# Performance work log

Hardware: AMD Instinct MI355X
Metric: run time of the kernel (lower is better)

Reference implementation:

```python
import jax, jax.numpy as jnp
import numpy as np

NALGOS = 64
NTASKS = 256
SEQLEN = 4096


def setup_inputs() -> dict:
    key = jax.random.key(0)
    k1, k2, k3, k4, k5, k6 = jax.random.split(key, 6)
    lx = jax.random.randint(k1, (SEQLEN,), 0, NTASKS)
    task_matrix = jax.random.uniform(k2, (NTASKS, NTASKS), jnp.float32) * 2.0 - 1.0
    # positive, bounded away from zero (module clamps difficulty to >= 0)
    task_difficulty = jax.random.uniform(k3, (NTASKS,), jnp.float32) + 0.5
    alg_efficiency = 0.5 + 0.02 * jax.random.normal(k4, (NALGOS,), jnp.float32)
    alg_memory = 0.5 + 0.10 * jax.random.normal(k5, (NALGOS,), jnp.float32)
    alg_experience_boost = 0.5 + 0.02 * jax.random.normal(k6, (NALGOS,), jnp.float32)
    return {
        "lx": lx,
        "task_matrix": task_matrix,
        "task_difficulty": task_difficulty,
        "alg_efficiency": alg_efficiency,
        "alg_memory": alg_memory,
        "alg_experience_boost": alg_experience_boost,
    }


def _custom_sigmoid(x):
    # 2*exp(x)/(exp(x)+1) - 1  ==  2*sigmoid(x) - 1 (stable form)
    return 2.0 * jax.nn.sigmoid(x) - 1.0


def reference(lx, task_matrix, task_difficulty, alg_efficiency, alg_memory,
              alg_experience_boost):
    nalgos = alg_efficiency.shape[0]
    ntasks = task_matrix.shape[0]
    task_difficulty_scale = 1.0
    difficulty = task_difficulty * task_difficulty_scale  # (T,)

    mem = alg_memory[:, None]              # (A, 1)
    eff = alg_efficiency[:, None]          # (A, 1)
    boost = alg_experience_boost[:, None]  # (A, 1)

    def step(carry, t):
        res, sig = carry                   # each (A, T)
        tm_row = task_matrix[t][None, :]   # (1, T): transfer from current task t
        sig_task = sig[:, t][:, None]      # (A, 1): prior perf on current task
        new_res = res * mem + tm_row * (eff + sig_task * boost)
        new_sig = _custom_sigmoid(new_res / difficulty[None, :])
        return (new_res, new_sig), new_sig

    init = (jnp.zeros((nalgos, ntasks), task_matrix.dtype),
            jnp.zeros((nalgos, ntasks), task_matrix.dtype))
    _, sigs = jax.lax.scan(step, init, lx)        # (S, A, T)
    sigs = jnp.moveaxis(sigs, 0, -1)              # (A, T, S)
    # prepend the zero initial state at timestep 0 -> (A, T, S+1)
    zero0 = jnp.zeros((nalgos, ntasks, 1), sigs.dtype)
    return jnp.concatenate([zero0, sigs], axis=-1)
```

## Files before the change

kernel.cpp:

```cpp
#include <hip/hip_runtime.h>

#define SEQ 4096
#define NT  256
#define NA  64
#define NCKPT 16
#define LOG2E 1.4426950408889634f

__device__ __forceinline__ float rdlanef(float v, int l) {
    return __int_as_float(__builtin_amdgcn_readlane(__float_as_int(v), l));
}

__global__ __launch_bounds__(64) void k_chain(
    const int* __restrict__ lx, const float* __restrict__ tm,
    const float* __restrict__ diff, const float* __restrict__ eff_p,
    const float* __restrict__ mem_p, const float* __restrict__ boost_p,
    float* __restrict__ gbuf, float* __restrict__ ckpt)
{
    __shared__ int   s_lx[SEQ + 8];
    __shared__ float s_res[NT];
    const int lane = threadIdx.x;
    const int a = blockIdx.x;

    for (int i = lane; i < SEQ; i += 64) s_lx[i] = lx[i];
    if (lane < 8) s_lx[SEQ + lane] = lx[SEQ - 1];
    *(float4*)&s_res[4 * lane] = make_float4(0.f, 0.f, 0.f, 0.f);
    __syncthreads();

    const float eff   = eff_p[a];
    const float mem   = mem_p[a];
    const float boost = boost_p[a];
    const float A  = eff + boost;
    const float Bc = -2.0f * boost;

    float mpow = 1.0f, bb = mem;
    {
        const int n = 63 - lane;
#pragma unroll
        for (int k = 0; k < 6; ++k) { if (n & (1 << k)) mpow *= bb; bb *= bb; }
    }
    const float m64 = bb;

    float4 res = make_float4(0.0f, 0.0f, 0.0f, 0.0f);
    float g = eff;
    float garr = g;
    float T[64];

    int   vrow  = s_lx[lane];
    int   vcol  = s_lx[1 + lane];
    float klane = LOG2E / diff[vcol];
    float D = 0.0f;
#pragma unroll
    for (int i = 0; i < 64; ++i) {
        const int r = __builtin_amdgcn_readlane(vrow, i);
        T[i] = klane * tm[r * NT + vcol];
    }

    for (int B = 0; B < SEQ; B += 64) {
#pragma unroll
        for (int j = 0; j < 64; ++j) {
            garr = (lane == j) ? g : garr;
            const float tg = T[j] * g;
            D = fmaf(mem, D, tg);
            const float pb = rdlanef(D, j);
            const float q  = __builtin_amdgcn_rcpf(
                                 __builtin_amdgcn_exp2f(pb) + 1.0f);
            g = fmaf(Bc, q, A);
        }
        gbuf[a * SEQ + B + lane] = garr;

        const int Bn = B + 64;
        const bool last = (Bn >= SEQ);

        int vrow_n = vrow, vcol_n = vcol; float klane_n = klane;
        if (!last) {
            vrow_n  = s_lx[Bn + lane];
            vcol_n  = s_lx[Bn + 1 + lane];
            klane_n = LOG2E / diff[vcol_n];
#pragma unroll
            for (int i = 0; i < 64; ++i) {
                const int r = __builtin_amdgcn_readlane(vrow_n, i);
                T[i] = klane_n * tm[r * NT + vcol_n];
            }
        }

        const float w = garr * mpow;
        res.x *= m64; res.y *= m64; res.z *= m64; res.w *= m64;
        float4 pf[16];
#pragma unroll
        for (int d = 0; d < 16; ++d) {
            const int r = __builtin_amdgcn_readlane(vrow, d);
            pf[d] = *(const float4*)(tm + r * NT + 4 * lane);
        }
#pragma unroll
        for (int i = 0; i < 64; ++i) {
            const float sw = rdlanef(w, i);
            const float4 row = pf[i & 15];
            res.x = fmaf(sw, row.x, res.x);
            res.y = fmaf(sw, row.y, res.y);
            res.z = fmaf(sw, row.z, res.z);
            res.w = fmaf(sw, row.w, res.w);
            if (i < 48) {
                const int r = __builtin_amdgcn_readlane(vrow, i + 16);
                pf[i & 15] = *(const float4*)(tm + r * NT + 4 * lane);
            }
        }
        if ((Bn & 255) == 0)
            *(float4*)(ckpt + (a * NCKPT + (B >> 8)) * NT + 4 * lane) = res;

        if (!last) {
            __syncthreads();
            *(float4*)&s_res[4 * lane] = res;
            __syncthreads();
            const float R = s_res[vcol_n];
            D = klane_n * R;
            vrow = vrow_n; vcol = vcol_n; klane = klane_n;
        }
    }
}

__global__ __launch_bounds__(64) void k_out(
    const int* __restrict__ lx, const float* __restrict__ tm,
    const float* __restrict__ diff, const float* __restrict__ mem_p,
    const float* __restrict__ gbuf, const float* __restrict__ ckpt,
    float* __restrict__ out)
{
    __shared__ int   s_lx[256 + 8];
    __shared__ float s_g[256];
    __shared__ float s_tile[64 * 65];

    const int lane = threadIdx.x;
    const int b = blockIdx.x;
    const int a     = b >> 6;
    const int cg    = (b >> 4) & 3;
    const int chunk = b & 15;
    const int t0 = chunk << 8;

    for (int i = lane; i < 256; i += 64) {
        s_lx[i] = lx[t0 + i];
        s_g[i]  = gbuf[a * SEQ + t0 + i];
    }
    if (lane < 8) s_lx[256 + lane] = lx[t0 + 255];
    __syncthreads();

    const int c = (cg << 6) + lane;
    const float memv = mem_p[a];
    const float kc = LOG2E / diff[c];
    float res = (chunk == 0) ? 0.0f
                             : ckpt[(a * NCKPT + chunk - 1) * NT + c];

    float pf[8];
#pragma unroll
    for (int d = 0; d < 8; ++d) pf[d] = tm[s_lx[d] * NT + c];

    const long rowbase = (long)(a * NT + (cg << 6)) * (SEQ + 1);
    for (int jb = 0; jb < 256; jb += 64) {
        const int   vpfl = s_lx[jb + 8 + lane];
        const float vg   = s_g[jb + lane];
        for (int j0 = 0; j0 < 64; j0 += 8) {
#pragma unroll
            for (int ji = 0; ji < 8; ++ji) {
                const int j2 = j0 + ji;
                const float gi  = rdlanef(vg, j2);
                const float tmv = pf[ji];
                res = fmaf(memv, res, tmv * gi);
                const float q = __builtin_amdgcn_rcpf(
                                    __builtin_amdgcn_exp2f(res * kc) + 1.0f);
                s_tile[j2 * 65 + lane] = fmaf(-2.0f, q, 1.0f);
                const int rowi = __builtin_amdgcn_readlane(vpfl, j2);
                pf[ji] = tm[rowi * NT + c];
            }
        }
        __syncthreads();
        const int tbase = t0 + jb + 1;
#pragma unroll 8
        for (int r = 0; r < 64; ++r) {
            out[rowbase + (long)r * (SEQ + 1) + tbase + lane] =
                s_tile[lane * 65 + r];
        }
        __syncthreads();
    }
    if (chunk == 0) out[rowbase + (long)lane * (SEQ + 1)] = 0.0f;
}

extern "C" void kernel_launch(void* const* d_in, const int* in_sizes, int n_in,
                              void* d_out, int out_size, void* d_ws, size_t ws_size,
                              hipStream_t stream)
{
    const int*   lx    = (const int*)d_in[0];
    const float* tm    = (const float*)d_in[1];
    const float* diff  = (const float*)d_in[2];
    const float* eff   = (const float*)d_in[3];
    const float* memp  = (const float*)d_in[4];
    const float* boost = (const float*)d_in[5];
    float* gbuf = (float*)d_ws;
    float* ckpt = gbuf + NA * SEQ;
    float* out  = (float*)d_out;

    k_chain<<<NA, 64, 0, stream>>>(lx, tm, diff, eff, memp, boost, gbuf, ckpt);
    k_out<<<NA * 4 * NCKPT, 64, 0, stream>>>(lx, tm, diff, memp, gbuf, ckpt, out);
}
```

Measured before the change: 591.6 us.

## Split chain into serial-scan wave and full-row update wave with precomputed transfer tables

The per-algorithm chain kernel now runs two waves. Wave 0 runs the serial 64-step scan for block n. Wave 1 meanwhile applies block n-1's full 256-wide residual update, with double-buffered shared memory between them. Two new pre-kernels precompute the scaled transfer tables T and V (the next block's lookahead contribution) into workspace, so the serial wave no longer gathers them or waits on the full update before continuing. The output kernel is reindexed to emit sigmoid before the update, with a longer prefetch distance. This adds two launches and workspace traffic, and the chain's critical path now carries an extra FMA per step.

```diff
diff --git a/kernel.cpp b/kernel.cpp
--- a/kernel.cpp
+++ b/kernel.cpp
@@ -10,20 +10,75 @@
     return __int_as_float(__builtin_amdgcn_readlane(__float_as_int(v), l));
 }
 
-__global__ __launch_bounds__(64) void k_chain(
+__global__ __launch_bounds__(256) void k_prep(
+    const int* __restrict__ lx, const float* __restrict__ tm,
+    const float* __restrict__ diff, float* __restrict__ Tbuf)
+{
+    const int t   = threadIdx.x;
+    const int blk = blockIdx.x >> 2;
+    const int sub = blockIdx.x & 3;
+    const int j   = t & 63;
+    const int i0  = (sub * 4 + (t >> 6)) * 4;
+
+    int cjidx = 64 * blk + j + 1;
+    if (cjidx > SEQ - 1) cjidx = SEQ - 1;
+    const int   cj = lx[cjidx];
+    const float kj = LOG2E / diff[cj];
+    const float* src = tm + cj;
+    float4 v;
+    v.x = kj * src[lx[64 * blk + i0 + 0] * NT];
+    v.y = kj * src[lx[64 * blk + i0 + 1] * NT];
+    v.z = kj * src[lx[64 * blk + i0 + 2] * NT];
+    v.w = kj * src[lx[64 * blk + i0 + 3] * NT];
+    *(float4*)(Tbuf + ((blk * 16 + (i0 >> 2)) << 8) + 4 * j) = v;
+}
+
+__global__ __launch_bounds__(256) void k_prep2(
+    const int* __restrict__ lx, const float* __restrict__ tm,
+    const float* __restrict__ diff, float* __restrict__ Vbuf)
+{
+    const int t   = threadIdx.x;
+    const int n   = blockIdx.x >> 2;
+    const int sub = blockIdx.x & 3;
+    const int j   = t & 63;
+    const int i0  = (sub * 4 + (t >> 6)) * 4;
+
+    int cjidx = 64 * (n + 1) + j + 1;
+    if (cjidx > SEQ - 1) cjidx = SEQ - 1;
+    const int   cj = lx[cjidx];
+    const float kj = LOG2E / diff[cj];
+    const float* src = tm + cj;
+    float4 v;
+    v.x = kj * src[lx[64 * n + i0 + 0] * NT];
+    v.y = kj * src[lx[64 * n + i0 + 1] * NT];
+    v.z = kj * src[lx[64 * n + i0 + 2] * NT];
+    v.w = kj * src[lx[64 * n + i0 + 3] * NT];
+    *(float4*)(Vbuf + ((n * 16 + (i0 >> 2)) << 8) + 4 * j) = v;
+}
+
+__global__ __launch_bounds__(128, 1) void k_chain(
     const int* __restrict__ lx, const float* __restrict__ tm,
     const float* __restrict__ diff, const float* __restrict__ eff_p,
     const float* __restrict__ mem_p, const float* __restrict__ boost_p,
+    const float* __restrict__ Tbuf, const float* __restrict__ Vbuf,
     float* __restrict__ gbuf, float* __restrict__ ckpt)
 {
-    __shared__ int   s_lx[SEQ + 8];
-    __shared__ float s_res[NT];
-    const int lane = threadIdx.x;
-    const int a = blockIdx.x;
-
-    for (int i = lane; i < SEQ; i += 64) s_lx[i] = lx[i];
-    if (lane < 8) s_lx[SEQ + lane] = lx[SEQ - 1];
-    *(float4*)&s_res[4 * lane] = make_float4(0.f, 0.f, 0.f, 0.f);
+    __shared__ int   s_lx[SEQ + 16];
+    __shared__ float s_kd[NT];
+    __shared__ float s_res[2][NT];
+    __shared__ float s_g[2][64];
+
+    const int tid  = threadIdx.x;
+    const int lane = tid & 63;
+    const int w    = tid >> 6;
+    const int a    = blockIdx.x;
+
+    for (int i = tid; i < SEQ; i += 128) s_lx[i] = lx[i];
+    if (tid < 16) s_lx[SEQ + tid] = lx[SEQ - 1];
+    s_kd[tid]       = LOG2E / diff[tid];
+    s_kd[tid + 128] = LOG2E / diff[tid + 128];
+    s_res[0][tid] = 0.0f; s_res[0][tid + 128] = 0.0f;
+    s_res[1][tid] = 0.0f; s_res[1][tid + 128] = 0.0f;
     __syncthreads();
 
     const float eff   = eff_p[a];
@@ -31,90 +86,71 @@
     const float boost = boost_p[a];
     const float A  = eff + boost;
     const float Bc = -2.0f * boost;
-
-    float mpow = 1.0f, bb = mem;
-    {
-        const int n = 63 - lane;
-#pragma unroll
-        for (int k = 0; k < 6; ++k) { if (n & (1 << k)) mpow *= bb; bb *= bb; }
-    }
-    const float m64 = bb;
-
+    float m64 = mem;
+#pragma unroll
+    for (int k = 0; k < 6; ++k) m64 *= m64;
+
+    float T[64], V[64];
+    float D = 0.0f, vA = 0.0f, g = eff, garr = eff;
     float4 res = make_float4(0.0f, 0.0f, 0.0f, 0.0f);
-    float g = eff;
-    float garr = g;
-    float T[64];
-
-    int   vrow  = s_lx[lane];
-    int   vcol  = s_lx[1 + lane];
-    float klane = LOG2E / diff[vcol];
-    float D = 0.0f;
-#pragma unroll
-    for (int i = 0; i < 64; ++i) {
-        const int r = __builtin_amdgcn_readlane(vrow, i);
-        T[i] = klane * tm[r * NT + vcol];
-    }
-
-    for (int B = 0; B < SEQ; B += 64) {
-#pragma unroll
-        for (int j = 0; j < 64; ++j) {
-            garr = (lane == j) ? g : garr;
-            const float tg = T[j] * g;
-            D = fmaf(mem, D, tg);
-            const float pb = rdlanef(D, j);
-            const float q  = __builtin_amdgcn_rcpf(
-                                 __builtin_amdgcn_exp2f(pb) + 1.0f);
-            g = fmaf(Bc, q, A);
-        }
-        gbuf[a * SEQ + B + lane] = garr;
-
-        const int Bn = B + 64;
-        const bool last = (Bn >= SEQ);
-
-        int vrow_n = vrow, vcol_n = vcol; float klane_n = klane;
-        if (!last) {
-            vrow_n  = s_lx[Bn + lane];
-            vcol_n  = s_lx[Bn + 1 + lane];
-            klane_n = LOG2E / diff[vcol_n];
+    float4 pf[8];
+
+    for (int n = 0; n <= 64; ++n) {
+        if (w == 0 && n < 64) {
+            const float* tb = Tbuf + ((n * 16) << 8) + 4 * lane;
+            const float* vb = Vbuf + ((n * 16) << 8) + 4 * lane;
+#pragma unroll
+            for (int q = 0; q < 16; ++q) {
+                *(float4*)&T[4 * q] = *(const float4*)(tb + (q << 8));
+                if (n < 63)
+                    *(float4*)&V[4 * q] = *(const float4*)(vb + (q << 8));
+            }
+            const int   vcol = s_lx[64 * n + 1 + lane];
+            const float kp   = s_kd[vcol];
+            const float Rv   = s_res[n & 1][vcol];
+            D  = fmaf(kp * m64, Rv, vA);
+            vA = 0.0f;
+#pragma unroll
+            for (int j = 0; j < 64; ++j) {
+                garr = (lane == j) ? g : garr;
+                D  = fmaf(T[j], g, mem * D);
+                vA = fmaf(V[j], g, mem * vA);
+                const float pb = rdlanef(D, j);
+                const float q2 = __builtin_amdgcn_rcpf(
+                                     __builtin_amdgcn_exp2f(pb) + 1.0f);
+                g = fmaf(Bc, q2, A);
+            }
+            s_g[n & 1][lane] = garr;
+        }
+        if (w == 1 && n > 0) {
+            const int bm1 = n - 1;
+            const int S1  = bm1 << 6;
+            const float vg = s_g[bm1 & 1][lane];
+            gbuf[a * SEQ + S1 + lane] = vg;
+            const int vrow = s_lx[S1 + lane];
+#pragma unroll
+            for (int d = 0; d < 8; ++d) {
+                const int rr = __builtin_amdgcn_readlane(vrow, d);
+                pf[d] = *(const float4*)(tm + rr * NT + 4 * lane);
+            }
 #pragma unroll
             for (int i = 0; i < 64; ++i) {
-                const int r = __builtin_amdgcn_readlane(vrow_n, i);
-                T[i] = klane_n * tm[r * NT + vcol_n];
-            }
-        }
-
-        const float w = garr * mpow;
-        res.x *= m64; res.y *= m64; res.z *= m64; res.w *= m64;
-        float4 pf[16];
-#pragma unroll
-        for (int d = 0; d < 16; ++d) {
-            const int r = __builtin_amdgcn_readlane(vrow, d);
-            pf[d] = *(const float4*)(tm + r * NT + 4 * lane);
-        }
-#pragma unroll
-        for (int i = 0; i < 64; ++i) {
-            const float sw = rdlanef(w, i);
-            const float4 row = pf[i & 15];
-            res.x = fmaf(sw, row.x, res.x);
-            res.y = fmaf(sw, row.y, res.y);
-            res.z = fmaf(sw, row.z, res.z);
-            res.w = fmaf(sw, row.w, res.w);
-            if (i < 48) {
-                const int r = __builtin_amdgcn_readlane(vrow, i + 16);
-                pf[i & 15] = *(const float4*)(tm + r * NT + 4 * lane);
-            }
-        }
-        if ((Bn & 255) == 0)
-            *(float4*)(ckpt + (a * NCKPT + (B >> 8)) * NT + 4 * lane) = res;
-
-        if (!last) {
-            __syncthreads();
-            *(float4*)&s_res[4 * lane] = res;
-            __syncthreads();
-            const float R = s_res[vcol_n];
-            D = klane_n * R;
-            vrow = vrow_n; vcol = vcol_n; klane = klane_n;
-        }
+                const float gi = rdlanef(vg, i);
+                const float4 row = pf[i & 7];
+                res.x = fmaf(gi, row.x, mem * res.x);
+                res.y = fmaf(gi, row.y, mem * res.y);
+                res.z = fmaf(gi, row.z, mem * res.z);
+                res.w = fmaf(gi, row.w, mem * res.w);
+                if (i < 56) {
+                    const int rr = __builtin_amdgcn_readlane(vrow, i + 8);
+                    pf[i & 7] = *(const float4*)(tm + rr * NT + 4 * lane);
+                }
+            }
+            *(float4*)&s_res[bm1 & 1][4 * lane] = res;
+            if ((bm1 & 3) == 3)
+                *(float4*)(ckpt + (a * NCKPT + (bm1 >> 2)) * NT + 4 * lane) = res;
+        }
+        __syncthreads();
     }
 }
 
@@ -124,7 +160,7 @@
     const float* __restrict__ gbuf, const float* __restrict__ ckpt,
     float* __restrict__ out)
 {
-    __shared__ int   s_lx[256 + 8];
+    __shared__ int   s_lx[256 + 16];
     __shared__ float s_g[256];
     __shared__ float s_tile[64 * 65];
 
@@ -139,7 +175,7 @@
         s_lx[i] = lx[t0 + i];
         s_g[i]  = gbuf[a * SEQ + t0 + i];
     }
-    if (lane < 8) s_lx[256 + lane] = lx[t0 + 255];
+    if (lane < 16) s_lx[256 + lane] = lx[t0 + 255];
     __syncthreads();
 
     const int c = (cg << 6) + lane;
@@ -148,30 +184,31 @@
     float res = (chunk == 0) ? 0.0f
                              : ckpt[(a * NCKPT + chunk - 1) * NT + c];
 
-    float pf[8];
-#pragma unroll
-    for (int d = 0; d < 8; ++d) pf[d] = tm[s_lx[d] * NT + c];
+    float pf[16];
+#pragma unroll
+    for (int d = 0; d < 16; ++d) pf[d] = tm[s_lx[d] * NT + c];
 
     const long rowbase = (long)(a * NT + (cg << 6)) * (SEQ + 1);
     for (int jb = 0; jb < 256; jb += 64) {
-        const int   vpfl = s_lx[jb + 8 + lane];
-        const float vg   = s_g[jb + lane];
+        const float vg  = s_g[jb + lane];
+        const int   vpf = s_lx[jb + 16 + lane];
         for (int j0 = 0; j0 < 64; j0 += 8) {
 #pragma unroll
             for (int ji = 0; ji < 8; ++ji) {
                 const int j2 = j0 + ji;
-                const float gi  = rdlanef(vg, j2);
-                const float tmv = pf[ji];
-                res = fmaf(memv, res, tmv * gi);
+                const int i  = jb + j2;
                 const float q = __builtin_amdgcn_rcpf(
                                     __builtin_amdgcn_exp2f(res * kc) + 1.0f);
                 s_tile[j2 * 65 + lane] = fmaf(-2.0f, q, 1.0f);
-                const int rowi = __builtin_amdgcn_readlane(vpfl, j2);
-                pf[ji] = tm[rowi * NT + c];
+                const float gi  = rdlanef(vg, j2);
+                const float tmv = pf[i & 15];
+                res = fmaf(memv, res, tmv * gi);
+                const int rowi = __builtin_amdgcn_readlane(vpf, j2);
+                pf[i & 15] = tm[rowi * NT + c];
             }
         }
         __syncthreads();
-        const int tbase = t0 + jb + 1;
+        const int tbase = t0 + jb;
 #pragma unroll 8
         for (int r = 0; r < 64; ++r) {
             out[rowbase + (long)r * (SEQ + 1) + tbase + lane] =
@@ -179,7 +216,11 @@
         }
         __syncthreads();
     }
-    if (chunk == 0) out[rowbase + (long)lane * (SEQ + 1)] = 0.0f;
+    if (chunk == 15) {
+        const float q = __builtin_amdgcn_rcpf(
+                            __builtin_amdgcn_exp2f(res * kc) + 1.0f);
+        out[rowbase + (long)lane * (SEQ + 1) + SEQ] = fmaf(-2.0f, q, 1.0f);
+    }
 }
 
 extern "C" void kernel_launch(void* const* d_in, const int* in_sizes, int n_in,
@@ -194,8 +235,13 @@
     const float* boost = (const float*)d_in[5];
     float* gbuf = (float*)d_ws;
     float* ckpt = gbuf + NA * SEQ;
+    float* Tbuf = ckpt + NA * NCKPT * NT;
+    float* Vbuf = Tbuf + 64 * 64 * 64;
     float* out  = (float*)d_out;
 
-    k_chain<<<NA, 64, 0, stream>>>(lx, tm, diff, eff, memp, boost, gbuf, ckpt);
-    k_out<<<NA * 4 * NCKPT, 64, 0, stream>>>(lx, tm, diff, memp, gbuf, ckpt, out);
-}
+    k_prep <<<256, 256, 0, stream>>>(lx, tm, diff, Tbuf);
+    k_prep2<<<252, 256, 0, stream>>>(lx, tm, diff, Vbuf);
+    k_chain<<<NA, 128, 0, stream>>>(lx, tm, diff, eff, memp, boost,
+                                    Tbuf, Vbuf, gbuf, ckpt);
+    k_out  <<<NA * 4 * NCKPT, 64, 0, stream>>>(lx, tm, diff, memp, gbuf, ckpt, out);
+}
```

Result: faster. 483.6 us (-18.2%).
